# Optimization experiments

Hardware: AMD Instinct MI355X
Metric: run time of the kernel (lower is better)

Reference implementation:

```python
import jax, jax.numpy as jnp
import numpy as np
import math

DIM = 1024
N_HEADS = 16
N_KV_HEADS = 8
HEAD_DIM = 64
HIDDEN = 4096
WINDOW = 512
NORM_EPS = 1e-5
QK_EPS = 1e-6


def get_alibi_slopes(n_heads):
    def _power_of_2(n):
        start = 2 ** (-2 ** (-(math.log2(n) - 3)))
        return [start * start ** i for i in range(n)]
    if math.log2(n_heads).is_integer():
        return _power_of_2(n_heads)
    closest = 2 ** math.floor(math.log2(n_heads))
    slopes = _power_of_2(closest)
    extra = _power_of_2(2 * closest)
    slopes.extend(extra[0::2][:n_heads - closest])
    return slopes


def layer_norm(x, w, eps):
    m = x.mean(-1, keepdims=True)
    v = ((x - m) ** 2).mean(-1, keepdims=True)
    return (x - m) * jax.lax.rsqrt(v + eps) * w


def setup_inputs() -> dict:
    key = jax.random.key(0)
    ks = jax.random.split(key, 16)
    s = 0.02
    return {
        "x": jax.random.normal(ks[0], (2, 2048, DIM), dtype=jnp.float32),
        "wq": jax.random.normal(ks[1], (N_HEADS * HEAD_DIM, DIM), dtype=jnp.float32) * s,
        "wk": jax.random.normal(ks[2], (N_KV_HEADS * HEAD_DIM, DIM), dtype=jnp.float32) * s,
        "wv": jax.random.normal(ks[3], (N_KV_HEADS * HEAD_DIM, DIM), dtype=jnp.float32) * s,
        "wo": jax.random.normal(ks[4], (DIM, N_HEADS * HEAD_DIM), dtype=jnp.float32) * s,
        "q_norm_w": jnp.ones((N_HEADS * HEAD_DIM,), dtype=jnp.float32),
        "k_norm_w": jnp.ones((N_KV_HEADS * HEAD_DIM,), dtype=jnp.float32),
        "attn_norm_w": jnp.ones((DIM,), dtype=jnp.float32),
        "ffn_norm_w": jnp.ones((DIM,), dtype=jnp.float32),
        "w1": jax.random.normal(ks[5], (HIDDEN, DIM), dtype=jnp.float32) * s,
        "w2": jax.random.normal(ks[6], (DIM, HIDDEN), dtype=jnp.float32) * s,
        "w3": jax.random.normal(ks[7], (HIDDEN, DIM), dtype=jnp.float32) * s,
        "attn_scale": jnp.full((DIM,), 1e-5, dtype=jnp.float32),
        "ffn_scale": jnp.full((DIM,), 1e-5, dtype=jnp.float32),
    }


def reference(x, wq, wk, wv, wo, q_norm_w, k_norm_w, attn_norm_w, ffn_norm_w,
              w1, w2, w3, attn_scale, ffn_scale):
    bsz, seqlen, _ = x.shape
    n_rep = N_HEADS // N_KV_HEADS

    h = layer_norm(x, attn_norm_w, NORM_EPS)
    q = layer_norm(h @ wq.T, q_norm_w, QK_EPS).reshape(bsz, seqlen, N_HEADS, HEAD_DIM).transpose(0, 2, 1, 3)
    k = layer_norm(h @ wk.T, k_norm_w, QK_EPS).reshape(bsz, seqlen, N_KV_HEADS, HEAD_DIM).transpose(0, 2, 1, 3)
    v = (h @ wv.T).reshape(bsz, seqlen, N_KV_HEADS, HEAD_DIM).transpose(0, 2, 1, 3)
    k = jnp.repeat(k, n_rep, axis=1)  # [b, H, s, hd]
    v = jnp.repeat(v, n_rep, axis=1)

    pos = jnp.arange(seqlen)
    dist = pos[None, :] - pos[:, None]  # dist[i, j] = j - i (as in the torch code)
    base = jnp.where((dist >= 0) & (dist <= WINDOW), 0.0, -jnp.inf)  # [s, s]
    slopes = jnp.asarray(get_alibi_slopes(N_HEADS), dtype=jnp.float32)
    alibi = -jnp.abs(slopes[:, None, None] * dist.astype(jnp.float32))  # [H, s, s]
    full_mask = base[None, :, :] + alibi  # [H, s, s]

    scores = jnp.einsum('bhqd,bhkd->bhqk', q, k) / math.sqrt(HEAD_DIM) + full_mask[None]
    attn = jax.nn.softmax(scores, axis=-1)
    out = jnp.einsum('bhqk,bhkd->bhqd', attn, v)
    out = out.transpose(0, 2, 1, 3).reshape(bsz, seqlen, N_HEADS * HEAD_DIM)
    x = x + (out @ wo.T) * attn_scale

    h2 = layer_norm(x, ffn_norm_w, NORM_EPS)
    ffn = (jax.nn.silu(h2 @ w1.T) * (h2 @ w3.T)) @ w2.T
    return x + ffn * ffn_scale
```

## Files before the change

### kernel.cpp

```cpp
#include <hip/hip_runtime.h>


typedef __bf16 bf16;
typedef __attribute__((ext_vector_type(8))) __bf16 bf16x8;
typedef __attribute__((ext_vector_type(4))) float f32x4;
typedef __attribute__((ext_vector_type(4))) short s16x4;

#define MFMA16(a, b, c) __builtin_amdgcn_mfma_f32_16x16x32_bf16(a, b, c, 0, 0, 0)

__device__ __forceinline__ void gload_lds16(const bf16* g, bf16* l) {
    __builtin_amdgcn_global_load_lds(
        (const __attribute__((address_space(1))) unsigned int*)g,
        (__attribute__((address_space(3))) unsigned int*)l, 16, 0, 0);
}

__global__ void sniff_kernel(const unsigned short* __restrict__ x, int* __restrict__ flag) {
    __shared__ int s;
    if (threadIdx.x == 0) s = 0;
    __syncthreads();
    int bad = 0;
#pragma unroll
    for (int i = 0; i < 16; ++i) {
        const unsigned short u = x[threadIdx.x * 16 + i];
        const int e = (u >> 7) & 0xFF;
        if (e >= 135) bad = 1;
    }
    if (bad) atomicOr(&s, 1);
    __syncthreads();
    if (threadIdx.x == 0) flag[0] = s;
}

__global__ void convert_all_kernel(const void* __restrict__ wq, const void* __restrict__ wk,
                                   const void* __restrict__ wv, const void* __restrict__ wo,
                                   const void* __restrict__ w1, const void* __restrict__ w3,
                                   const void* __restrict__ w2, bf16* __restrict__ dst,
                                   const int* __restrict__ flag) {
    const long e = ((long)blockIdx.x * 256 + threadIdx.x) * 4;
    const void* src; long off;
    if      (e < 1048576)  { src = wq; off = 0; }
    else if (e < 1572864)  { src = wk; off = 1048576; }
    else if (e < 2097152)  { src = wv; off = 1572864; }
    else if (e < 3145728)  { src = wo; off = 2097152; }
    else if (e < 7340032)  { src = w1; off = 3145728; }
    else if (e < 11534336) { src = w3; off = 7340032; }
    else                   { src = w2; off = 11534336; }
    if (flag[0] != 0) {
        const f32x4 v = *(const f32x4*)((const float*)src + (e - off));
        bf16 tmp[4];
#pragma unroll
        for (int j = 0; j < 4; ++j) tmp[j] = (bf16)v[j];
        *(s16x4*)(dst + e) = *(s16x4*)tmp;
    } else {
        *(s16x4*)(dst + e) = *(const s16x4*)((const short*)src + (e - off));
    }
}

__global__ void ln_kernel(const void* __restrict__ in, const void* __restrict__ w,
                          bf16* __restrict__ out, int W, float eps,
                          const int* __restrict__ flag, int in_flv, int w_flv) {
    const int row = blockIdx.x, t = threadIdx.x;
    const int nch = W >> 3;
    const bool act = t < nch;
    const bool f32 = flag[0] != 0;
    float v[8];
    float s = 0.f, s2 = 0.f;
    if (act) {
        if (in_flv && f32) {
            const float* rp = (const float*)in + (size_t)row * W + t * 8;
            const f32x4 a = *(const f32x4*)rp, b = *(const f32x4*)(rp + 4);
#pragma unroll
            for (int j = 0; j < 4; ++j) { v[j] = a[j]; v[4 + j] = b[j]; }
        } else {
            const bf16x8 xv = *(const bf16x8*)((const bf16*)in + (size_t)row * W + t * 8);
#pragma unroll
            for (int j = 0; j < 8; ++j) v[j] = (float)xv[j];
        }
#pragma unroll
        for (int j = 0; j < 8; ++j) { s += v[j]; s2 += v[j] * v[j]; }
    }
#pragma unroll
    for (int off = 32; off; off >>= 1) { s += __shfl_xor(s, off); s2 += __shfl_xor(s2, off); }
    __shared__ float red[4];
    if ((t & 63) == 0) { red[(t >> 6) * 2] = s; red[(t >> 6) * 2 + 1] = s2; }
    __syncthreads();
    const float fs = red[0] + red[2], fs2 = red[1] + red[3];
    const float inw = 1.f / (float)W;
    const float mean = fs * inw;
    const float var = fs2 * inw - mean * mean;
    const float rstd = rsqrtf(var + eps);
    if (act) {
        float wv8[8];
        if (w_flv && f32) {
            const float* wp = (const float*)w + t * 8;
            const f32x4 a = *(const f32x4*)wp, b = *(const f32x4*)(wp + 4);
#pragma unroll
            for (int j = 0; j < 4; ++j) { wv8[j] = a[j]; wv8[4 + j] = b[j]; }
        } else {
            const bf16x8 ww = *(const bf16x8*)((const bf16*)w + t * 8);
#pragma unroll
            for (int j = 0; j < 8; ++j) wv8[j] = (float)ww[j];
        }
        bf16x8 ov;
#pragma unroll
        for (int j = 0; j < 8; ++j) ov[j] = (bf16)((v[j] - mean) * rstd * wv8[j]);
        *(bf16x8*)(out + (size_t)row * W + t * 8) = ov;
    }
}

template <int EPI, int NBUF, int SWZ>
__global__ __launch_bounds__(512, 4)
void gemm2(const bf16* __restrict__ A, const bf16* __restrict__ B,
           void* __restrict__ Cout, const void* __restrict__ res,
           const void* __restrict__ scale, int M, int N, int K,
           const int* __restrict__ flag, int res_flv, int out_flv) {
    __shared__ bf16 LDS[NBUF * 8192];
    const bool f32 = flag[0] != 0;
    const int t = threadIdx.x;
    const int wv = t >> 6, ln = t & 63;
    const int qr = ln & 15, g = ln >> 4;
    const int wr = wv >> 2, wc = wv & 3;
    int bx = blockIdx.x, by = blockIdx.y;
    if (SWZ) {
        const int bid = by * gridDim.x + bx;
        const int g8 = bid & 7, m = bid >> 3;
        bx = m % gridDim.x;
        by = g8 + 8 * (m / gridDim.x);
    }
    const int row0 = by * 128, col0 = bx * 128;

    f32x4 acc[4][2] = {};

    const int cx = ((t & 3) ^ ((t >> 2) & 3)) * 8;
    const bf16* aSrc = A + (size_t)(row0 + (t >> 2)) * K + cx;
    const bf16* bSrc = B + (size_t)(col0 + (t >> 2)) * K + cx;
    const int gx8 = (g ^ (qr & 3)) * 8;
    const int NIT = K >> 5;

#define STAGE(bi, k0)                                              \
    do {                                                           \
        bf16* lb = LDS + (bi) * 8192 + wv * 512;                   \
        gload_lds16(aSrc + (k0), lb);                              \
        gload_lds16(bSrc + (k0), lb + 4096);                       \
    } while (0)

#pragma unroll
    for (int pb = 0; pb < NBUF - 1; ++pb) STAGE(pb, pb * 32);
    if constexpr (NBUF == 3) asm volatile("s_waitcnt vmcnt(2)" ::: "memory");
    else                     asm volatile("s_waitcnt vmcnt(6)" ::: "memory");
    __builtin_amdgcn_s_barrier();
    __builtin_amdgcn_sched_barrier(0);

    int cur = 0, sb = NBUF - 1;
    for (int it = 0; it < NIT; ++it) {
        const bool more = (it + NBUF - 1) < NIT;
        if (more) STAGE(sb, (it + NBUF - 1) * 32);
        const bf16* bufA = LDS + cur * 8192;
        const bf16* bufB = bufA + 4096;
        bf16x8 af[4], bfr[2];
#pragma unroll
        for (int i = 0; i < 4; ++i)
            af[i] = *(const bf16x8*)&bufA[(wr * 64 + i * 16 + qr) * 32 + gx8];
#pragma unroll
        for (int j = 0; j < 2; ++j)
            bfr[j] = *(const bf16x8*)&bufB[(wc * 32 + j * 16 + qr) * 32 + gx8];
#pragma unroll
        for (int i = 0; i < 4; ++i)
#pragma unroll
            for (int j = 0; j < 2; ++j)
                acc[i][j] = MFMA16(af[i], bfr[j], acc[i][j]);
        if (more) {
            if constexpr (NBUF == 3) asm volatile("s_waitcnt vmcnt(2)" ::: "memory");
            else                     asm volatile("s_waitcnt vmcnt(6)" ::: "memory");
        } else {
            asm volatile("s_waitcnt vmcnt(0)" ::: "memory");
        }
        __builtin_amdgcn_s_barrier();
        __builtin_amdgcn_sched_barrier(0);
        cur = cur + 1 == NBUF ? 0 : cur + 1;
        sb  = sb + 1 == NBUF ? 0 : sb + 1;
    }
#undef STAGE

#pragma unroll
    for (int i = 0; i < 4; ++i) {
#pragma unroll
        for (int j = 0; j < 2; ++j) {
            const int rr0 = row0 + wr * 64 + i * 16 + g * 4;
            const int cc  = col0 + wc * 32 + j * 16 + qr;
            if (EPI == 4) {
                if (cc < 1024) {
#pragma unroll
                    for (int r = 0; r < 4; ++r)
                        ((bf16*)Cout)[(size_t)(rr0 + r) * 1024 + cc] = (bf16)acc[i][j][r];
                } else if (cc < 1536) {
#pragma unroll
                    for (int r = 0; r < 4; ++r)
                        ((bf16*)res)[(size_t)(rr0 + r) * 512 + (cc - 1024)] = (bf16)acc[i][j][r];
                } else {
                    const int kv = cc - 1536, kvh = kv >> 6, d = kv & 63;
                    const int bb = rr0 >> 11, s0 = rr0 & 2047;
                    bf16 tmp[4];
#pragma unroll
                    for (int r = 0; r < 4; ++r) tmp[r] = (bf16)acc[i][j][r];
                    *(s16x4*)((bf16*)scale + (((size_t)bb * 8 + kvh) * 64 + d) * 2048 + s0) = *(s16x4*)tmp;
                }
            } else {
                float scv = 0.f;
                if (EPI == 1)
                    scv = f32 ? ((const float*)scale)[cc] : (float)((const bf16*)scale)[cc];
#pragma unroll
                for (int r = 0; r < 4; ++r) {
                    const size_t idx = (size_t)(rr0 + r) * N + cc;
                    float vv = acc[i][j][r];
                    if (EPI == 1) {
                        const float rv = (res_flv && f32) ? ((const float*)res)[idx]
                                                          : (float)((const bf16*)res)[idx];
                        vv = rv + vv * scv;
                    }
                    if (EPI == 3) {
                        const float uv = (float)((const bf16*)res)[idx];
                        vv = uv / (1.f + __expf(-uv)) * vv;
                    }
                    if (out_flv && f32) ((float*)Cout)[idx] = vv;
                    else                ((bf16*)Cout)[idx] = (bf16)vv;
                }
            }
        }
    }
}

template <int EPI>
__global__ __launch_bounds__(512, 4)
void gemm3(const bf16* __restrict__ A, const bf16* __restrict__ B,
           bf16* __restrict__ C, const bf16* __restrict__ res,
           int M, int N, int K) {
    __shared__ bf16 LDS[3 * 12288];
    const int t = threadIdx.x;
    const int wv = t >> 6, ln = t & 63;
    const int qr = ln & 15, g = ln >> 4;
    const int wr = wv >> 1, wc = wv & 1;
    const int row0 = blockIdx.y * 256, col0 = blockIdx.x * 128;

    f32x4 acc[4][4] = {};

    const int cx = ((t & 3) ^ ((t >> 2) & 3)) * 8;
    const bf16* aSrc  = A + (size_t)(row0 + (t >> 2)) * K + cx;
    const bf16* aSrc2 = A + (size_t)(row0 + 128 + (t >> 2)) * K + cx;
    const bf16* bSrc  = B + (size_t)(col0 + (t >> 2)) * K + cx;
    const int gx8 = (g ^ (qr & 3)) * 8;
    const int NIT = K >> 5;

#define STAGE3(bi, k0)                                             \
    do {                                                           \
        bf16* lb = LDS + (bi) * 12288 + wv * 512;                  \
        gload_lds16(aSrc + (k0), lb);                              \
        gload_lds16(aSrc2 + (k0), lb + 4096);                      \
        gload_lds16(bSrc + (k0), lb + 8192);                       \
    } while (0)

    STAGE3(0, 0);
    STAGE3(1, 32);
    asm volatile("s_waitcnt vmcnt(3)" ::: "memory");
    __builtin_amdgcn_s_barrier();
    __builtin_amdgcn_sched_barrier(0);

    int cur = 0, sb = 2;
    for (int it = 0; it < NIT; ++it) {
        const bool more = (it + 2) < NIT;
        if (more) STAGE3(sb, (it + 2) * 32);
        const bf16* bufA = LDS + cur * 12288;
        const bf16* bufB = bufA + 8192;
        bf16x8 af[4], bfr[4];
#pragma unroll
        for (int i = 0; i < 4; ++i)
            af[i] = *(const bf16x8*)&bufA[(wr * 64 + i * 16 + qr) * 32 + gx8];
#pragma unroll
        for (int j = 0; j < 4; ++j)
            bfr[j] = *(const bf16x8*)&bufB[(wc * 64 + j * 16 + qr) * 32 + gx8];
#pragma unroll
        for (int i = 0; i < 4; ++i)
#pragma unroll
            for (int j = 0; j < 4; ++j)
                acc[i][j] = MFMA16(bfr[j], af[i], acc[i][j]);
        if (more) asm volatile("s_waitcnt vmcnt(3)" ::: "memory");
        else      asm volatile("s_waitcnt vmcnt(0)" ::: "memory");
        __builtin_amdgcn_s_barrier();
        __builtin_amdgcn_sched_barrier(0);
        cur = cur == 2 ? 0 : cur + 1;
        sb  = sb  == 2 ? 0 : sb  + 1;
    }
#undef STAGE3

#pragma unroll
    for (int i = 0; i < 4; ++i) {
        const int row = row0 + wr * 64 + i * 16 + qr;
#pragma unroll
        for (int j = 0; j < 4; ++j) {
            const int col = col0 + wc * 64 + j * 16 + g * 4;
            const size_t idx = (size_t)row * N + col;
            bf16 tmp[4];
            if (EPI == 3) {
                const s16x4 rv4 = *(const s16x4*)(res + idx);
#pragma unroll
                for (int r = 0; r < 4; ++r) {
                    bf16 ub; *(short*)&ub = rv4[r];
                    const float uv = (float)ub;
                    tmp[r] = (bf16)(uv / (1.f + __expf(-uv)) * acc[i][j][r]);
                }
            } else {
#pragma unroll
                for (int r = 0; r < 4; ++r) tmp[r] = (bf16)acc[i][j][r];
            }
            *(s16x4*)(C + idx) = *(s16x4*)tmp;
        }
    }
}

__global__ __launch_bounds__(256)
void attn_kernel(const bf16* __restrict__ qn, const bf16* __restrict__ kn,
                 const bf16* __restrict__ vt, bf16* __restrict__ aout) {
    __shared__ bf16 SH[3 * 4096];
    const int t = threadIdx.x, wv = t >> 6, ln = t & 63;
    const int qr = ln & 15, g = ln >> 4;
    const int h = blockIdx.y, b = blockIdx.z, kvh = h >> 1;
    const int q0blk = blockIdx.x * 64;
    const int qa = q0blk + wv * 16 + qr;
    const float slope = exp2f(-0.5f * (float)(h + 1));

    const bf16* qrow = qn + ((size_t)(b * 2048 + qa)) * 1024 + h * 64;
    const bf16x8 qb0 = *(const bf16x8*)(qrow + g * 8);
    const bf16x8 qb1 = *(const bf16x8*)(qrow + 32 + g * 8);

    const bf16* kbase = kn + (size_t)b * 2048 * 512 + kvh * 64;
    const bf16* vbase = vt + ((size_t)(b * 8 + kvh) * 64) * 2048;
    const int krow_l = t >> 3;
    const int kcsrc  = (t & 7) ^ ((t >> 3) & 7);
    const int vd     = t >> 2;
    const int vcsrc  = (t & 3) ^ ((t >> 2) & 3);
    const bf16* kgsrc = kbase + kcsrc * 8;
    const bf16* vgsrc = vbase + (size_t)vd * 2048;
    bf16* lK0 = SH + wv * 512;
    bf16* lV0 = SH + 2048 + wv * 512;

#define STAGE_T(kts, bi)                                           \
    do {                                                           \
        int ksrc = (kts) + krow_l;                                 \
        ksrc = ksrc > 2047 ? 2047 : ksrc;                          \
        gload_lds16(kgsrc + (size_t)ksrc * 512, lK0 + (bi) * 4096);\
        int vsrc = (kts) + vcsrc * 8;                              \
        vsrc = vsrc > 2040 ? 2040 : vsrc;                          \
        gload_lds16(vgsrc + vsrc, lV0 + (bi) * 4096);              \
    } while (0)

    STAGE_T(q0blk, 0);
    STAGE_T(q0blk + 32, 1);
    STAGE_T(q0blk + 64, 2);
    asm volatile("s_waitcnt vmcnt(4)" ::: "memory");
    __builtin_amdgcn_s_barrier();
    __builtin_amdgcn_sched_barrier(0);

    f32x4 o[4] = {};
    float mrun = -1e29f, lsum = 0.f;
    int cur = 0;

    for (int it = 0; it < 18; ++it) {
        const int kt = q0blk + it * 32;
        const bf16* Kb = SH + cur * 4096;
        const bf16* Vb = Kb + 2048;

        f32x4 sc[2] = {f32x4{0, 0, 0, 0}, f32x4{0, 0, 0, 0}};
#pragma unroll
        for (int ks = 0; ks < 2; ++ks) {
            const int lrow = ks * 16 + qr;
            const int sw = (lrow & 7) * 8;
            sc[ks] = MFMA16(*(const bf16x8*)&Kb[lrow * 64 + (((g) * 8) ^ sw)],        qb0, sc[ks]);
            sc[ks] = MFMA16(*(const bf16x8*)&Kb[lrow * 64 + (((4 + g) * 8) ^ sw)],    qb1, sc[ks]);
        }
        float s[2][4], p[2][4];
        float tmax = -1e30f;
#pragma unroll
        for (int ks = 0; ks < 2; ++ks)
#pragma unroll
            for (int r = 0; r < 4; ++r) {
                const int key = kt + ks * 16 + g * 4 + r;
                const int dist = key - qa;
                const bool valid = (dist >= 0) && (dist <= 512) && (key < 2048);
                const float sv = valid ? sc[ks][r] * 0.125f - slope * (float)dist : -1e30f;
                s[ks][r] = sv;
                tmax = fmaxf(tmax, sv);
            }
        tmax = fmaxf(tmax, __shfl_xor(tmax, 16));
        tmax = fmaxf(tmax, __shfl_xor(tmax, 32));
        const float mnew = fmaxf(mrun, tmax);
        const float alpha = __expf(mrun - mnew);
        mrun = mnew;
        float ps = 0.f;
#pragma unroll
        for (int ks = 0; ks < 2; ++ks)
#pragma unroll
            for (int r = 0; r < 4; ++r) { p[ks][r] = __expf(s[ks][r] - mnew); ps += p[ks][r]; }
        lsum = lsum * alpha + ps;
#pragma unroll
        for (int fd = 0; fd < 4; ++fd) o[fd] *= alpha;

        bf16x8 pb;
#pragma unroll
        for (int j = 0; j < 8; ++j) {
            const int srcl = (((2 * g + (j >> 2)) & 3) << 4) | qr;
            const float v0 = __shfl(p[0][j & 3], srcl);
            const float v1 = __shfl(p[1][j & 3], srcl);
            pb[j] = (bf16)((g & 2) ? v1 : v0);
        }
#pragma unroll
        for (int fd = 0; fd < 4; ++fd) {
            const int d = fd * 16 + qr;
            const bf16x8 va = *(const bf16x8*)&Vb[d * 32 + ((g ^ (d & 3)) * 8)];
            o[fd] = MFMA16(va, pb, o[fd]);
        }

        __builtin_amdgcn_s_barrier();
        if (it + 3 < 18) {
            STAGE_T(kt + 96, cur);
            asm volatile("s_waitcnt vmcnt(4)" ::: "memory");
        } else {
            asm volatile("s_waitcnt vmcnt(0)" ::: "memory");
        }
        __builtin_amdgcn_s_barrier();
        __builtin_amdgcn_sched_barrier(0);
        cur = cur == 2 ? 0 : cur + 1;
    }
#undef STAGE_T

    float lt = lsum + __shfl_xor(lsum, 16);
    lt += __shfl_xor(lt, 32);
    lt = fmaxf(lt, 1e-30f);
    const float inv = 1.f / lt;
    bf16* orow = aout + ((size_t)(b * 2048 + qa)) * 1024 + h * 64;
#pragma unroll
    for (int fd = 0; fd < 4; ++fd) {
        bf16 tmp[4];
#pragma unroll
        for (int r = 0; r < 4; ++r) tmp[r] = (bf16)(o[fd][r] * inv);
        *(s16x4*)(orow + fd * 16 + g * 4) = *(s16x4*)tmp;
    }
}

extern "C" void kernel_launch(void* const* d_in, const int* in_sizes, int n_in,
                              void* d_out, int out_size, void* d_ws, size_t ws_size,
                              hipStream_t stream) {
    int* flag = (int*)d_ws;
    bf16* base = (bf16*)d_ws + 64;
    bf16* h    = base;
    bf16* q    = h + 4194304;
    bf16* kbuf = q + 4194304;
    bf16* vtb  = kbuf + 2097152;
    bf16* aout = vtb + 2097152;
    bf16* u    = aout + 4194304;
    bf16* wcv  = u + 16777216;

    bf16* woc = wcv + 2097152;
    bf16* w1c = wcv + 3145728;
    bf16* w3c = wcv + 7340032;
    bf16* w2c = wcv + 11534336;

    const dim3 blk(512);
    sniff_kernel<<<1, 256, 0, stream>>>((const unsigned short*)d_in[0], flag);
    convert_all_kernel<<<15360, 256, 0, stream>>>(
        d_in[1], d_in[2], d_in[3], d_in[4], d_in[9], d_in[11], d_in[10], wcv, flag);

    ln_kernel<<<4096, 128, 0, stream>>>(d_in[0], d_in[7], h, 1024, 1e-5f, flag, 1, 1);
    gemm2<4, 3, 0><<<dim3(16, 32), blk, 0, stream>>>(h, wcv, q, kbuf, vtb, 4096, 2048, 1024, flag, 0, 0);
    ln_kernel<<<4096, 128, 0, stream>>>(q, d_in[5], q, 1024, 1e-6f, flag, 0, 1);
    ln_kernel<<<4096, 128, 0, stream>>>(kbuf, d_in[6], kbuf, 512, 1e-6f, flag, 0, 1);
    attn_kernel<<<dim3(32, 16, 2), dim3(256), 0, stream>>>(q, kbuf, vtb, aout);
    gemm2<1, 3, 1><<<dim3(8, 32), blk, 0, stream>>>(aout, woc, q, d_in[0], d_in[12], 4096, 1024, 1024, flag, 1, 0);
    ln_kernel<<<4096, 128, 0, stream>>>(q, d_in[8], h, 1024, 1e-5f, flag, 0, 1);
    gemm3<0><<<dim3(32, 16), blk, 0, stream>>>(h, w1c, u, nullptr, 4096, 4096, 1024);
    gemm3<3><<<dim3(32, 16), blk, 0, stream>>>(h, w3c, u, u,       4096, 4096, 1024);
    gemm2<1, 5, 1><<<dim3(8, 32), blk, 0, stream>>>(u, w2c, d_out, q, d_in[13], 4096, 1024, 4096, flag, 0, 1);
}
```

Measured before the change: 272.6 us.

## Split-K the down-projection GEMM and restructure attention K/V prefetch

The final FFN down-projection GEMM (K=4096, only 256 blocks) is split into two K halves across blockIdx.z. Each half writes bf16 partials into the reused kbuf/vtb scratch, and a new reduce_k kernel sums them, applies ffn_scale and adds the residual. This is meant to raise occupancy on a grid too small to fill the GPU, at the cost of extra partial-sum memory traffic, one more launch, and bf16 rounding of the partials. Separately, the attention loop now issues the next tile prefetch at the top of each iteration, with two tiles in flight instead of three, and drops one barrier per iteration.

Result: faster. 267.1 us (-2.0%).

```diff
diff --git a/kernel.cpp b/kernel.cpp
--- a/kernel.cpp
+++ b/kernel.cpp
@@ -107,7 +107,45 @@
     }
 }
 
-template <int EPI, int NBUF, int SWZ>
+__global__ void reduce_k(const bf16* __restrict__ p, const bf16* __restrict__ x1,
+                         const void* __restrict__ scale, void* __restrict__ out,
+                         const int* __restrict__ flag) {
+    const bool f32 = flag[0] != 0;
+    const size_t i8 = ((size_t)blockIdx.x * 256 + threadIdx.x) * 8;
+    const int col = (int)(i8 & 1023);
+    const bf16x8 a = *(const bf16x8*)(p + i8);
+    const bf16x8 b = *(const bf16x8*)(p + 4194304 + i8);
+    const bf16x8 r = *(const bf16x8*)(x1 + i8);
+    float sc8[8];
+    if (f32) {
+        const f32x4 s0 = *(const f32x4*)((const float*)scale + col);
+        const f32x4 s1 = *(const f32x4*)((const float*)scale + col + 4);
+#pragma unroll
+        for (int j = 0; j < 4; ++j) { sc8[j] = s0[j]; sc8[4 + j] = s1[j]; }
+    } else {
+        const bf16x8 sb = *(const bf16x8*)((const bf16*)scale + col);
+#pragma unroll
+        for (int j = 0; j < 8; ++j) sc8[j] = (float)sb[j];
+    }
+    float o[8];
+#pragma unroll
+    for (int j = 0; j < 8; ++j)
+        o[j] = (float)r[j] + ((float)a[j] + (float)b[j]) * sc8[j];
+    if (f32) {
+        f32x4 o0, o1;
+#pragma unroll
+        for (int j = 0; j < 4; ++j) { o0[j] = o[j]; o1[j] = o[4 + j]; }
+        *(f32x4*)((float*)out + i8) = o0;
+        *(f32x4*)((float*)out + i8 + 4) = o1;
+    } else {
+        bf16x8 ov;
+#pragma unroll
+        for (int j = 0; j < 8; ++j) ov[j] = (bf16)o[j];
+        *(bf16x8*)((bf16*)out + i8) = ov;
+    }
+}
+
+template <int EPI, int NBUF, int SWZ, int SPLITK>
 __global__ __launch_bounds__(512, 4)
 void gemm2(const bf16* __restrict__ A, const bf16* __restrict__ B,
            void* __restrict__ Cout, const void* __restrict__ res,
@@ -128,13 +166,17 @@
     }
     const int row0 = by * 128, col0 = bx * 128;
 
+    const int Koff = SPLITK ? (int)blockIdx.z * (K >> 1) : 0;
+    const int Keff = SPLITK ? (K >> 1) : K;
+    if (SPLITK) Cout = (void*)((bf16*)Cout + (size_t)blockIdx.z * ((size_t)M * N));
+
     f32x4 acc[4][2] = {};
 
     const int cx = ((t & 3) ^ ((t >> 2) & 3)) * 8;
-    const bf16* aSrc = A + (size_t)(row0 + (t >> 2)) * K + cx;
-    const bf16* bSrc = B + (size_t)(col0 + (t >> 2)) * K + cx;
+    const bf16* aSrc = A + (size_t)(row0 + (t >> 2)) * K + Koff + cx;
+    const bf16* bSrc = B + (size_t)(col0 + (t >> 2)) * K + Koff + cx;
     const int gx8 = (g ^ (qr & 3)) * 8;
-    const int NIT = K >> 5;
+    const int NIT = Keff >> 5;
 
 #define STAGE(bi, k0)                                              \
     do {                                                           \
@@ -354,17 +396,18 @@
 
     STAGE_T(q0blk, 0);
     STAGE_T(q0blk + 32, 1);
-    STAGE_T(q0blk + 64, 2);
-    asm volatile("s_waitcnt vmcnt(4)" ::: "memory");
+    asm volatile("s_waitcnt vmcnt(2)" ::: "memory");
     __builtin_amdgcn_s_barrier();
     __builtin_amdgcn_sched_barrier(0);
 
     f32x4 o[4] = {};
     float mrun = -1e29f, lsum = 0.f;
-    int cur = 0;
+    int cur = 0, sb = 2;
 
     for (int it = 0; it < 18; ++it) {
         const int kt = q0blk + it * 32;
+        const bool more = (it + 2) < 18;
+        if (more) STAGE_T(kt + 64, sb);
         const bf16* Kb = SH + cur * 4096;
         const bf16* Vb = Kb + 2048;
 
@@ -418,16 +461,12 @@
             o[fd] = MFMA16(va, pb, o[fd]);
         }
 
-        __builtin_amdgcn_s_barrier();
-        if (it + 3 < 18) {
-            STAGE_T(kt + 96, cur);
-            asm volatile("s_waitcnt vmcnt(4)" ::: "memory");
-        } else {
-            asm volatile("s_waitcnt vmcnt(0)" ::: "memory");
-        }
+        if (more) asm volatile("s_waitcnt vmcnt(2)" ::: "memory");
+        else      asm volatile("s_waitcnt vmcnt(0)" ::: "memory");
         __builtin_amdgcn_s_barrier();
         __builtin_amdgcn_sched_barrier(0);
         cur = cur == 2 ? 0 : cur + 1;
+        sb  = sb  == 2 ? 0 : sb  + 1;
     }
 #undef STAGE_T
 
@@ -469,13 +508,14 @@
         d_in[1], d_in[2], d_in[3], d_in[4], d_in[9], d_in[11], d_in[10], wcv, flag);
 
     ln_kernel<<<4096, 128, 0, stream>>>(d_in[0], d_in[7], h, 1024, 1e-5f, flag, 1, 1);
-    gemm2<4, 3, 0><<<dim3(16, 32), blk, 0, stream>>>(h, wcv, q, kbuf, vtb, 4096, 2048, 1024, flag, 0, 0);
+    gemm2<4, 3, 0, 0><<<dim3(16, 32), blk, 0, stream>>>(h, wcv, q, kbuf, vtb, 4096, 2048, 1024, flag, 0, 0);
     ln_kernel<<<4096, 128, 0, stream>>>(q, d_in[5], q, 1024, 1e-6f, flag, 0, 1);
     ln_kernel<<<4096, 128, 0, stream>>>(kbuf, d_in[6], kbuf, 512, 1e-6f, flag, 0, 1);
     attn_kernel<<<dim3(32, 16, 2), dim3(256), 0, stream>>>(q, kbuf, vtb, aout);
-    gemm2<1, 3, 1><<<dim3(8, 32), blk, 0, stream>>>(aout, woc, q, d_in[0], d_in[12], 4096, 1024, 1024, flag, 1, 0);
+    gemm2<1, 3, 1, 0><<<dim3(8, 32), blk, 0, stream>>>(aout, woc, q, d_in[0], d_in[12], 4096, 1024, 1024, flag, 1, 0);
     ln_kernel<<<4096, 128, 0, stream>>>(q, d_in[8], h, 1024, 1e-5f, flag, 0, 1);
     gemm3<0><<<dim3(32, 16), blk, 0, stream>>>(h, w1c, u, nullptr, 4096, 4096, 1024);
     gemm3<3><<<dim3(32, 16), blk, 0, stream>>>(h, w3c, u, u,       4096, 4096, 1024);
-    gemm2<1, 5, 1><<<dim3(8, 32), blk, 0, stream>>>(u, w2c, d_out, q, d_in[13], 4096, 1024, 4096, flag, 0, 1);
-}
+    gemm2<0, 5, 1, 1><<<dim3(8, 32, 2), blk, 0, stream>>>(u, w2c, kbuf, nullptr, nullptr, 4096, 1024, 4096, flag, 0, 0);
+    reduce_k<<<2048, 256, 0, stream>>>(kbuf, q, d_in[13], d_out, flag);
+}
```
